# Kernel optimization log

Hardware: AMD Instinct MI355X
Metric: run time of the kernel (lower is better)

The kernel has to match this reference:

```python
import jax, jax.numpy as jnp
import numpy as np

L = 1000  # fixed waveform length implied by MaxPool1d(1000) and [:, :, :1000] slices


def _conv1d(x, w, pad, reflect=False):
    # x: [B, Cin, T], w: [Cout, Cin, K]; torch conv1d == cross-correlation == lax conv
    if reflect:
        x = jnp.pad(x, ((0, 0), (0, 0), (pad, pad)), mode='reflect')
        pads = [(0, 0)]
    else:
        pads = [(pad, pad)]
    return jax.lax.conv_general_dilated(x, w, (1,), pads,
                                        dimension_numbers=('NCH', 'OIH', 'NCH'))


def setup_inputs() -> dict:
    key = jax.random.key(0)
    ks = jax.random.split(key, 10)
    B = 4096
    s = 0.1  # weight init scale
    return {
        'wf': jax.random.normal(ks[0], (B, 1, L), jnp.float32),
        'mask': jnp.ones((B, L), jnp.float32),
        'SPE': jax.random.uniform(ks[1], (L,), jnp.float32),
        'w_cum_area': jax.random.normal(ks[2], (1, 1, 121), jnp.float32) * s,
        'w_x': jax.random.normal(ks[3], (1, 1, 121), jnp.float32) * s,
        'w_div': jax.random.normal(ks[4], (1, 1, 121), jnp.float32) * s,
        'w_roll': jax.random.normal(ks[5], (1, 1, 101), jnp.float32) * s,
        'w_sub': jax.random.normal(ks[6], (15, 3, 21), jnp.float32) * s,
        'w_comb': jax.random.normal(ks[7], (1, 1, 5, 101, 3), jnp.float32) * s,
        'W_param': jnp.array([0.0, 5.0, 10.0], jnp.float32),
    }


def reference(wf, mask, SPE, w_cum_area, w_x, w_div, w_roll, w_sub, w_comb, W_param):
    B = wf.shape[0]
    # fixed (non-learned) derivative + running-mean kernels from __init__
    div_x_w = jnp.array([1/280, -4/105, 1/5, -4/5, 0.0, 4/5, -1/5, 4/105, -1/280],
                        jnp.float32).reshape(1, 1, 9)
    run_mean_w = jnp.full((1, 1, 51), 1.0 / 51, jnp.float32)

    # h = MaxPool1d(1000)(wf).squeeze(1).tile(1,3) / SPE.amax(); tiling == broadcast
    h = wf.max(axis=(1, 2))[:, None] / SPE.max()            # [B,1]
    W = jax.nn.softmax(-jax.nn.relu(h - W_param), axis=1)   # [B,3]

    cum_area = jnp.cumsum(wf, axis=-1)                      # [B,1,L]
    div_x_smd = _conv1d(_conv1d(wf, div_x_w, 4), run_mean_w, 25)  # zero-padded convs

    BL = _conv1d(cum_area, w_roll, 100, reflect=True)[:, :, :L] * w_cum_area.sum()
    fit_cum = jax.nn.relu(_conv1d(cum_area, w_cum_area, 100, reflect=True)[:, :, :L] - BL)
    fit_x = jax.nn.relu(_conv1d(wf, w_x, 100, reflect=True))[:, :, :L]
    fit_div = jax.nn.relu(_conv1d(div_x_smd, w_div, 100, reflect=True))[:, :, :L]

    features1 = jnp.concatenate([fit_cum, fit_x, fit_div], axis=1)   # [B,3,L]
    S = features1.sum(axis=2, keepdims=True) + 1e-10
    features1_norm = features1 / S

    features2 = _conv1d(features1_norm, w_sub, 10, reflect=True)     # [B,15,L]
    # [B,L,15] -> [B,L,5,3], weight the 3-way split by per-sample W
    fc = features2.transpose(0, 2, 1).reshape(B, L, 5, 3) * W[:, None, None, :]
    fc = fc.transpose(0, 2, 1, 3)[:, None]                           # [B,1,5,L,3]

    out = jax.lax.conv_general_dilated(fc, w_comb, (1, 1, 1),
                                       [(0, 0), (50, 50), (0, 0)],
                                       dimension_numbers=('NCDHW', 'OIDHW', 'NCDHW'))
    out = jax.nn.softplus(out).reshape(B, L)                         # [B,L]

    amax = out.max(axis=1, keepdims=True) + 1e-10
    out_norm = out / amax * mask
    return jax.nn.softmax(1e4 * out_norm, axis=1)
```

## Files before the change

kernel.cpp:

```cpp
#include <hip/hip_runtime.h>
#include <math.h>

#define TPB 256
#define LW  1000
#define CSTR 1124

#define OFF_WFE   0
#define OFF_CUME  1120
#define OFF_DSE   2240
#define OFF_F1E   3360
#define OFF_SCAND 3360
#define OFF_C     3872
#define OFF_RED   6740
#define SMEM_F    6748
#define OFF_KC    0
#define OFF_WS2   376
#define OFF_F2V   1456
#define OFF_PART  0

__device__ __forceinline__ float4 ld4(const float* p) { return *(const float4*)p; }

__device__ __forceinline__ float blk_red_max(float v, float* red) {
  #pragma unroll
  for (int o = 32; o > 0; o >>= 1) v = fmaxf(v, __shfl_xor(v, o, 64));
  const int w = threadIdx.x >> 6;
  if ((threadIdx.x & 63) == 0) red[w] = v;
  __syncthreads();
  float r = fmaxf(fmaxf(red[0], red[1]), fmaxf(red[2], red[3]));
  __syncthreads();
  return r;
}

__device__ __forceinline__ float blk_red_sum(float v, float* red) {
  #pragma unroll
  for (int o = 32; o > 0; o >>= 1) v += __shfl_xor(v, o, 64);
  const int w = threadIdx.x >> 6;
  if ((threadIdx.x & 63) == 0) red[w] = v;
  __syncthreads();
  float r = red[0] + red[1] + red[2] + red[3];
  __syncthreads();
  return r;
}

__device__ __forceinline__ int refl(int j) {
  return j < 0 ? -j : (j >= LW ? 2 * LW - 2 - j : j);
}

template<int OFF0>
__device__ __forceinline__ void f2v_accum(const float* xr, const float* wr, float acc[4]) {
  float xw[12];
  *(float4*)xw       = ld4(xr);
  *(float4*)(xw + 4) = ld4(xr + 4);
  *(float4*)(xw + 8) = ld4(xr + 8);
  #pragma unroll
  for (int jb = 0; jb < 20; jb += 4) {
    float4 w4 = ld4(wr + jb);
    const float wv[4] = {w4.x, w4.y, w4.z, w4.w};
    #pragma unroll
    for (int kk = 0; kk < 4; ++kk)
      #pragma unroll
      for (int o = 0; o < 4; ++o)
        acc[o] = fmaf(wv[kk], xw[OFF0 + kk + o], acc[o]);
    #pragma unroll
    for (int j = 0; j < 8; ++j) xw[j] = xw[j + 4];
    *(float4*)(xw + 8) = ld4(xr + jb + 12);
  }
  const float w20 = wr[20];
  #pragma unroll
  for (int o = 0; o < 4; ++o) acc[o] = fmaf(w20, xw[OFF0 + o], acc[o]);
}

extern "C" __global__ void prep_kernel(const float* __restrict__ wsub_g,
                                       const float* __restrict__ wcb_g,
                                       const float* __restrict__ wca_g,
                                       const float* __restrict__ spe_g,
                                       float* __restrict__ P) {
  __shared__ float sred[4];
  const int task = blockIdx.x * blockDim.x + threadIdx.x;
  if (task < 1089) {
    const int m = task / 363;
    const int r = task - m * 363;
    const int cin = r / 121;
    const int k = r - cin * 121;
    float acc = 0.f;
    for (int q = 0; q < 5; ++q) {
      const int ch = 3 * q + m;
      const float* ws = wsub_g + (ch * 3 + cin) * 21;
      #pragma unroll
      for (int j = 0; j < 21; ++j) {
        const int a = k - j;
        if (a >= 0 && a <= 100) acc = fmaf(ws[j], wcb_g[q * 303 + a * 3 + m], acc);
      }
    }
    P[task] = acc;
  } else if (task == 1089) {
    float s = 0.f;
    for (int k = 0; k < 121; ++k) s += wca_g[k];
    P[1089] = s;
  }
  if (blockIdx.x == 4) {
    float mx = -INFINITY;
    for (int t = threadIdx.x; t < LW; t += TPB) mx = fmaxf(mx, spe_g[t]);
    #pragma unroll
    for (int o = 32; o > 0; o >>= 1) mx = fmaxf(mx, __shfl_xor(mx, o, 64));
    if ((threadIdx.x & 63) == 0) sred[threadIdx.x >> 6] = mx;
    __syncthreads();
    if (threadIdx.x == 0)
      P[1090] = fmaxf(fmaxf(sred[0], sred[1]), fmaxf(sred[2], sred[3]));
  }
}

extern "C" __global__ void __launch_bounds__(TPB, 6)
spot_kernel(const float* __restrict__ wf_g,  const float* __restrict__ mask_g,
            const float* __restrict__ spe_g, const float* __restrict__ wca_g,
            const float* __restrict__ wx_g,  const float* __restrict__ wdv_g,
            const float* __restrict__ wrl_g, const float* __restrict__ wsub_g,
            const float* __restrict__ wcb_g, const float* __restrict__ wp_g,
            const float* __restrict__ P_g,   float* __restrict__ out_g)
{
  __shared__ __align__(16) float sm[SMEM_F];
  const int tid = threadIdx.x;
  const int b = blockIdx.x;
  const float* wf = wf_g + (size_t)b * LW;
  float* red = sm + OFF_RED;
  const int t0 = 4 * tid;

  for (int i = tid; i < 1120; i += TPB) sm[OFF_WFE + i] = wf[refl(i - 100)];
  double* scand = (double*)(sm + OFF_SCAND);
  double l0 = 0, l1 = 0, l2 = 0, l3 = 0;
  float hmx = -INFINITY;
  if (tid < 250) {
    float4 wv4 = ld4(wf + t0);
    hmx = fmaxf(fmaxf(wv4.x, wv4.y), fmaxf(wv4.z, wv4.w));
    l0 = (double)wv4.x;
    l1 = l0 + (double)wv4.y;
    l2 = l1 + (double)wv4.z;
    l3 = l2 + (double)wv4.w;
  }
  scand[tid] = l3;
  hmx = blk_red_max(hmx, red);

  const float smx = P_g[1090];
  const float swca = P_g[1089];
  const float h = hmx / smx;
  float a0 = -fmaxf(h - wp_g[0], 0.f);
  float a1 = -fmaxf(h - wp_g[1], 0.f);
  float a2 = -fmaxf(h - wp_g[2], 0.f);
  float am = fmaxf(a0, fmaxf(a1, a2));
  float e0 = expf(a0 - am), e1 = expf(a1 - am), e2 = expf(a2 - am);
  float es = e0 + e1 + e2;
  float Wv[3] = { e0 / es, e1 / es, e2 / es };

  if (tid < 64) {
    double s0 = scand[4 * tid], s1 = scand[4 * tid + 1];
    double s2 = scand[4 * tid + 2], s3 = scand[4 * tid + 3];
    double tot = s0 + s1 + s2 + s3;
    double inc = tot;
    #pragma unroll
    for (int o = 1; o < 64; o <<= 1) {
      double n = __shfl_up(inc, o, 64);
      if ((tid & 63) >= o) inc += n;
    }
    double ex = inc - tot;
    scand[4 * tid]     = ex;
    scand[4 * tid + 1] = ex + s0;
    scand[4 * tid + 2] = ex + s0 + s1;
    scand[4 * tid + 3] = ex + s0 + s1 + s2;
  }
  __syncthreads();
  if (tid < 250) {
    double base = scand[tid];
    float4 cv = { (float)(base + l0), (float)(base + l1),
                  (float)(base + l2), (float)(base + l3) };
    *(float4*)(sm + OFF_CUME + 100 + t0) = cv;
  }
  const float dker[9] = {1.f/280.f, -4.f/105.f, 0.2f, -0.8f, 0.f, 0.8f, -0.2f, 4.f/105.f, -1.f/280.f};
  float dv0 = 0, dv1 = 0, dv2 = 0, dv3 = 0;
  if (tid >= 1 && tid <= 248) {
    float xw[12];
    const float* xr = sm + OFF_WFE + t0 + 96;
    *(float4*)xw = ld4(xr); *(float4*)(xw+4) = ld4(xr+4); *(float4*)(xw+8) = ld4(xr+8);
    float d[4];
    #pragma unroll
    for (int j = 0; j < 4; ++j) {
      float a = 0.f;
      #pragma unroll
      for (int k = 0; k < 9; ++k) {
        if (k == 4) continue;
        a = fmaf(dker[k], xw[j + k], a);
      }
      d[j] = a;
    }
    dv0 = d[0]; dv1 = d[1]; dv2 = d[2]; dv3 = d[3];
  } else if (tid == 0 || tid == 249) {
    float d[4];
    #pragma unroll
    for (int j = 0; j < 4; ++j) {
      float a = 0.f;
      for (int k = 0; k < 9; ++k) {
        if (k == 4) continue;
        const int o = t0 + j - 4 + k;
        if (o >= 0 && o < LW) a = fmaf(dker[k], sm[OFF_WFE + 100 + o], a);
      }
      d[j] = a;
    }
    dv0 = d[0]; dv1 = d[1]; dv2 = d[2]; dv3 = d[3];
  }
  {
    const float s0 = dv0, s1 = s0 + dv1, s2 = s1 + dv2, s3 = s2 + dv3;
    float inc = s3;
    const int lane = tid & 63;
    #pragma unroll
    for (int o = 1; o < 64; o <<= 1) {
      float n = __shfl_up(inc, o, 64);
      if (lane >= o) inc += n;
    }
    float* redw = red + 4;
    if (lane == 63) redw[tid >> 6] = inc;
    __syncthreads();
    float base = 0.f;
    for (int w = 0; w < (tid >> 6); ++w) base += redw[w];
    if (tid < 250) {
      const float ex = base + inc - s3;
      float4 cv = { ex + s0, ex + s1, ex + s2, ex + s3 };
      *(float4*)(sm + OFF_C + t0) = cv;
    }
  }
  __syncthreads();
  for (int t = tid; t < LW; t += TPB) {
    const float hi = sm[OFF_C + (t + 25 > 999 ? 999 : t + 25)];
    const float lo = (t >= 26) ? sm[OFF_C + t - 26] : 0.f;
    sm[OFF_DSE + 100 + t] = (hi - lo) * (1.f / 51.f);
  }
  for (int i = tid; i < 120; i += TPB) {
    if (i < 100) sm[OFF_CUME + i] = sm[OFF_CUME + 200 - i];
    else         sm[OFF_CUME + 1000 + i] = sm[OFF_CUME + 2198 - (1000 + i)];
  }
  __syncthreads();
  for (int i = tid; i < 120; i += TPB) {
    if (i < 100) sm[OFF_DSE + i] = sm[OFF_DSE + 200 - i];
    else         sm[OFF_DSE + 1000 + i] = sm[OFF_DSE + 2198 - (1000 + i)];
  }
  __syncthreads();

  float lsC = 0.f, lsX = 0.f, lsD = 0.f;
  if (tid < 250) {
    const float* ce = sm + OFF_CUME + t0;
    const float* we = sm + OFF_WFE + t0;
    const float* de = sm + OFF_DSE + t0;
    float cw_[8], ww_[8], dw_[8];
    *(float4*)cw_ = ld4(ce); *(float4*)(cw_ + 4) = ld4(ce + 4);
    *(float4*)ww_ = ld4(we); *(float4*)(ww_ + 4) = ld4(we + 4);
    *(float4*)dw_ = ld4(de); *(float4*)(dw_ + 4) = ld4(de + 4);
    float aC[4] = {0,0,0,0}, aB[4] = {0,0,0,0}, aX[4] = {0,0,0,0}, aD[4] = {0,0,0,0};
    for (int g = 0; g < 100; g += 4) {
      #pragma unroll
      for (int kk = 0; kk < 4; ++kk) {
        const int k = g + kk;
        const float wa = wca_g[k], wxk = wx_g[k], wdk = wdv_g[k], wr = wrl_g[k];
        #pragma unroll
        for (int j = 0; j < 4; ++j) {
          aC[j] = fmaf(wa,  cw_[kk + j], aC[j]);
          aB[j] = fmaf(wr,  cw_[kk + j], aB[j]);
          aX[j] = fmaf(wxk, ww_[kk + j], aX[j]);
          aD[j] = fmaf(wdk, dw_[kk + j], aD[j]);
        }
      }
      #pragma unroll
      for (int j = 0; j < 4; ++j) { cw_[j] = cw_[j+4]; ww_[j] = ww_[j+4]; dw_[j] = dw_[j+4]; }
      *(float4*)(cw_ + 4) = ld4(ce + g + 8);
      *(float4*)(ww_ + 4) = ld4(we + g + 8);
      *(float4*)(dw_ + 4) = ld4(de + g + 8);
    }
    {
      const float wr100 = wrl_g[100];
      #pragma unroll
      for (int j = 0; j < 4; ++j) aB[j] = fmaf(wr100, cw_[j], aB[j]);
    }
    for (int g = 100; g < 116; g += 4) {
      #pragma unroll
      for (int kk = 0; kk < 4; ++kk) {
        const int k = g + kk;
        const float wa = wca_g[k], wxk = wx_g[k], wdk = wdv_g[k];
        #pragma unroll
        for (int j = 0; j < 4; ++j) {
          aC[j] = fmaf(wa,  cw_[kk + j], aC[j]);
          aX[j] = fmaf(wxk, ww_[kk + j], aX[j]);
          aD[j] = fmaf(wdk, dw_[kk + j], aD[j]);
        }
      }
      #pragma unroll
      for (int j = 0; j < 4; ++j) { cw_[j] = cw_[j+4]; ww_[j] = ww_[j+4]; dw_[j] = dw_[j+4]; }
      *(float4*)(cw_ + 4) = ld4(ce + g + 8);
      *(float4*)(ww_ + 4) = ld4(we + g + 8);
      *(float4*)(dw_ + 4) = ld4(de + g + 8);
    }
    #pragma unroll
    for (int kk = 0; kk < 5; ++kk) {
      const int k = 116 + kk;
      const float wa = wca_g[k], wxk = wx_g[k], wdk = wdv_g[k];
      #pragma unroll
      for (int j = 0; j < 4; ++j) {
        aC[j] = fmaf(wa,  cw_[kk + j], aC[j]);
        aX[j] = fmaf(wxk, ww_[kk + j], aX[j]);
        aD[j] = fmaf(wdk, dw_[kk + j], aD[j]);
      }
    }
    float4 vC, vX, vD;
    float* pC = (float*)&vC; float* pX = (float*)&vX; float* pD = (float*)&vD;
    #pragma unroll
    for (int j = 0; j < 4; ++j) {
      float fc = fmaxf(fmaf(-aB[j], swca, aC[j]), 0.f);
      float fx = fmaxf(aX[j], 0.f);
      float fd = fmaxf(aD[j], 0.f);
      pC[j] = fc; pX[j] = fx; pD[j] = fd;
      lsC += fc; lsX += fx; lsD += fd;
    }
    *(float4*)(sm + OFF_F1E + 0 * CSTR + 60 + t0) = vC;
    *(float4*)(sm + OFF_F1E + 1 * CSTR + 60 + t0) = vX;
    *(float4*)(sm + OFF_F1E + 2 * CSTR + 60 + t0) = vD;
  }
  const float SC = blk_red_sum(lsC, red) + 1e-10f;
  const float SX = blk_red_sum(lsX, red) + 1e-10f;
  const float SD = blk_red_sum(lsD, red) + 1e-10f;
  {
    const float iC = 1.f / SC, iX = 1.f / SX, iD = 1.f / SD;
    for (int t = tid; t < LW; t += TPB) {
      sm[OFF_F1E + 0 * CSTR + 60 + t] *= iC;
      sm[OFF_F1E + 1 * CSTR + 60 + t] *= iX;
      sm[OFF_F1E + 2 * CSTR + 60 + t] *= iD;
    }
  }
  __syncthreads();

  for (int i = tid; i < 360; i += TPB) {
    const int c = i / 120, j = i - c * 120;
    const int dst = (j < 60) ? j : (1000 + j);
    const int src = (j < 60) ? (120 - j) : (1118 - j);
    sm[OFF_F1E + c * CSTR + dst] = sm[OFF_F1E + c * CSTR + src];
  }
  for (int i = tid; i < 363; i += TPB) {
    const int cin = i / 121, k = i - cin * 121;
    const float* Pp = P_g + cin * 121 + k;
    sm[OFF_KC + cin * 124 + k] =
        fmaf(Wv[0], Pp[0], fmaf(Wv[1], Pp[363], Wv[2] * Pp[726]));
  }
  for (int i = tid; i < 1080; i += TPB) {
    const int row = i / 24, k = i - row * 24;
    sm[OFF_WS2 + i] = (k < 21) ? wsub_g[row * 21 + k] : 0.f;
  }
  __syncthreads();

  float res[4] = {0, 0, 0, 0};
  if (tid < 250) {
    #pragma unroll
    for (int cin = 0; cin < 3; ++cin) {
      const float* xr = sm + OFF_F1E + cin * CSTR + t0;
      const float* kc = sm + OFF_KC + cin * 124;
      float xw[8];
      *(float4*)xw = ld4(xr); *(float4*)(xw + 4) = ld4(xr + 4);
      for (int g = 0; g < 120; g += 4) {
        float4 kw = ld4(kc + g);
        const float wv[4] = {kw.x, kw.y, kw.z, kw.w};
        #pragma unroll
        for (int kk = 0; kk < 4; ++kk)
          #pragma unroll
          for (int j = 0; j < 4; ++j) res[j] = fmaf(wv[kk], xw[kk + j], res[j]);
        #pragma unroll
        for (int j = 0; j < 4; ++j) xw[j] = xw[j + 4];
        *(float4*)(xw + 4) = ld4(xr + g + 8);
      }
      const float w120 = kc[120];
      #pragma unroll
      for (int j = 0; j < 4; ++j) res[j] = fmaf(w120, xw[j], res[j]);
    }
  }
  for (int task = tid; task < 390; task += TPB) {
    const int side = (task >= 195) ? 1 : 0;
    const int r = task - 195 * side;
    const int ch = r / 13;
    const int gl = r - 13 * ch;
    float acc[4] = {0, 0, 0, 0};
    const float* wrb = sm + OFF_WS2 + ch * 72;
    if (side == 0) {
      const int xb = 4 * gl;
      #pragma unroll
      for (int cin = 0; cin < 3; ++cin)
        f2v_accum<0>(sm + OFF_F1E + cin * CSTR + xb, wrb + cin * 24, acc);
    } else {
      const int xb = 1048 + 4 * gl;
      #pragma unroll
      for (int cin = 0; cin < 3; ++cin)
        f2v_accum<2>(sm + OFF_F1E + cin * CSTR + xb, wrb + cin * 24, acc);
    }
    const int dst = OFF_F2V + ch * 104 + side * 52 + 4 * gl;
    if (gl < 12) {
      float4 st = {acc[0], acc[1], acc[2], acc[3]};
      *(float4*)(sm + dst) = st;
    } else {
      sm[dst] = acc[0]; sm[dst + 1] = acc[1];
    }
  }
  __syncthreads();

  for (int task = tid; task < 500; task += TPB) {
    const int q = task / 100;
    const int tcol = task - q * 100;
    const float* f0 = sm + OFF_F2V + (3 * q) * 104;
    float acc = 0.f;
    if (tcol < 50) {
      const int t = tcol;
      for (int a = 0; a <= 49 - t; ++a) {
        const int up = t + a;
        const float* wb = wcb_g + q * 303 + a * 3;
        acc = fmaf(Wv[0] * wb[0], f0[up], acc);
        acc = fmaf(Wv[1] * wb[1], f0[104 + up], acc);
        acc = fmaf(Wv[2] * wb[2], f0[208 + up], acc);
      }
    } else {
      const int tp = tcol;
      for (int d = 0; d <= tp - 50; ++d) {
        const int up = tp - d + 2;
        const int a = 100 - d;
        const float* wb = wcb_g + q * 303 + a * 3;
        acc = fmaf(Wv[0] * wb[0], f0[up], acc);
        acc = fmaf(Wv[1] * wb[1], f0[104 + up], acc);
        acc = fmaf(Wv[2] * wb[2], f0[208 + up], acc);
      }
    }
    sm[OFF_PART + task] = acc;
  }
  __syncthreads();

  if (tid < 250 && (t0 < 52 || t0 >= 948)) {
    #pragma unroll
    for (int j = 0; j < 4; ++j) {
      const int t = t0 + j;
      if (t < 50) {
        float c = 0.f;
        #pragma unroll
        for (int q = 0; q < 5; ++q) c += sm[OFF_PART + q * 100 + t];
        res[j] -= c;
      } else if (t >= 950) {
        const int tc = t - 900;
        float c = 0.f;
        #pragma unroll
        for (int q = 0; q < 5; ++q) c += sm[OFF_PART + q * 100 + tc];
        res[j] -= c;
      }
    }
  }
  float sp[4];
  float lm = -INFINITY;
  if (tid < 250) {
    #pragma unroll
    for (int j = 0; j < 4; ++j) {
      const float z = res[j];
      sp[j] = fmaxf(z, 0.f) + log1pf(expf(-fabsf(z)));
      lm = fmaxf(lm, sp[j]);
    }
  }
  const float amax = blk_red_max(lm, red) + 1e-10f;
  float v4[4];
  float lm2 = -INFINITY;
  if (tid < 250) {
    const float4 mv = ld4(mask_g + (size_t)b * LW + t0);
    const float* mj = (const float*)&mv;
    const float ia = 1e4f / amax;
    #pragma unroll
    for (int j = 0; j < 4; ++j) {
      v4[j] = (sp[j] * ia) * mj[j];
      lm2 = fmaxf(lm2, v4[j]);
    }
  }
  const float m2 = blk_red_max(lm2, red);
  float ls = 0.f;
  float e4[4];
  if (tid < 250) {
    #pragma unroll
    for (int j = 0; j < 4; ++j) {
      e4[j] = expf(v4[j] - m2);
      ls += e4[j];
    }
  }
  const float S2 = blk_red_sum(ls, red);
  if (tid < 250) {
    const float invs = 1.f / S2;
    float4 st = { e4[0] * invs, e4[1] * invs, e4[2] * invs, e4[3] * invs };
    *(float4*)(out_g + (size_t)b * LW + t0) = st;
  }
}

extern "C" void kernel_launch(void* const* d_in, const int* in_sizes, int n_in,
                              void* d_out, int out_size, void* d_ws, size_t ws_size,
                              hipStream_t stream) {
  (void)n_in; (void)ws_size; (void)out_size;
  const float* wf   = (const float*)d_in[0];
  const float* mask = (const float*)d_in[1];
  const float* spe  = (const float*)d_in[2];
  const float* wca  = (const float*)d_in[3];
  const float* wx   = (const float*)d_in[4];
  const float* wdv  = (const float*)d_in[5];
  const float* wrl  = (const float*)d_in[6];
  const float* wsub = (const float*)d_in[7];
  const float* wcb  = (const float*)d_in[8];
  const float* wp   = (const float*)d_in[9];
  float* P = (float*)d_ws;
  const int B = in_sizes[0] / LW;
  hipLaunchKernelGGL(prep_kernel, dim3(5), dim3(TPB), 0, stream, wsub, wcb, wca, spe, P);
  hipLaunchKernelGGL(spot_kernel, dim3(B), dim3(TPB), 0, stream,
                     wf, mask, spe, wca, wx, wdv, wrl, wsub, wcb, wp, P, (float*)d_out);
}
```

Before: 283.8 us.

## Fold baseline conv into cum-area weights and fuse block reductions

```diff
diff --git a/kernel.cpp b/kernel.cpp
--- a/kernel.cpp
+++ b/kernel.cpp
@@ -12,7 +12,7 @@
 #define OFF_SCAND 3360
 #define OFF_C     3872
 #define OFF_RED   6740
-#define SMEM_F    6748
+#define SMEM_F    6752
 #define OFF_KC    0
 #define OFF_WS2   376
 #define OFF_F2V   1456
@@ -42,8 +42,20 @@
   return r;
 }
 
-__device__ __forceinline__ int refl(int j) {
-  return j < 0 ? -j : (j >= LW ? 2 * LW - 2 - j : j);
+__device__ __forceinline__ void blk_red_sum3(float& a, float& b, float& c, float* red) {
+  #pragma unroll
+  for (int o = 32; o > 0; o >>= 1) {
+    a += __shfl_xor(a, o, 64);
+    b += __shfl_xor(b, o, 64);
+    c += __shfl_xor(c, o, 64);
+  }
+  const int w = threadIdx.x >> 6;
+  if ((threadIdx.x & 63) == 0) { red[w] = a; red[4 + w] = b; red[8 + w] = c; }
+  __syncthreads();
+  a = red[0] + red[1] + red[2]  + red[3];
+  b = red[4] + red[5] + red[6]  + red[7];
+  c = red[8] + red[9] + red[10] + red[11];
+  __syncthreads();
 }
 
 template<int OFF0>
@@ -74,8 +86,10 @@
                                        const float* __restrict__ wcb_g,
                                        const float* __restrict__ wca_g,
                                        const float* __restrict__ spe_g,
+                                       const float* __restrict__ wrl_g,
                                        float* __restrict__ P) {
   __shared__ float sred[4];
+  __shared__ float s_swca;
   const int task = blockIdx.x * blockDim.x + threadIdx.x;
   if (task < 1089) {
     const int m = task / 363;
@@ -93,10 +107,6 @@
       }
     }
     P[task] = acc;
-  } else if (task == 1089) {
-    float s = 0.f;
-    for (int k = 0; k < 121; ++k) s += wca_g[k];
-    P[1089] = s;
   }
   if (blockIdx.x == 4) {
     float mx = -INFINITY;
@@ -104,9 +114,20 @@
     #pragma unroll
     for (int o = 32; o > 0; o >>= 1) mx = fmaxf(mx, __shfl_xor(mx, o, 64));
     if ((threadIdx.x & 63) == 0) sred[threadIdx.x >> 6] = mx;
+    if (threadIdx.x == 0) {
+      float s = 0.f;
+      for (int k = 0; k < 121; ++k) s += wca_g[k];
+      s_swca = s;
+    }
     __syncthreads();
     if (threadIdx.x == 0)
       P[1090] = fmaxf(fmaxf(sred[0], sred[1]), fmaxf(sred[2], sred[3]));
+    if (threadIdx.x < 121) {
+      const int k = threadIdx.x;
+      float w = 0.f;
+      if (k < 101) w = wrl_g[k];
+      P[1091 + k] = wca_g[k] - s_swca * w;
+    }
   }
 }
 
@@ -125,12 +146,12 @@
   float* red = sm + OFF_RED;
   const int t0 = 4 * tid;
 
-  for (int i = tid; i < 1120; i += TPB) sm[OFF_WFE + i] = wf[refl(i - 100)];
   double* scand = (double*)(sm + OFF_SCAND);
   double l0 = 0, l1 = 0, l2 = 0, l3 = 0;
   float hmx = -INFINITY;
   if (tid < 250) {
     float4 wv4 = ld4(wf + t0);
+    *(float4*)(sm + OFF_WFE + 100 + t0) = wv4;
     hmx = fmaxf(fmaxf(wv4.x, wv4.y), fmaxf(wv4.z, wv4.w));
     l0 = (double)wv4.x;
     l1 = l0 + (double)wv4.y;
@@ -140,8 +161,12 @@
   scand[tid] = l3;
   hmx = blk_red_max(hmx, red);
 
+  for (int i = tid; i < 120; i += TPB) {
+    if (i < 100) sm[OFF_WFE + i] = sm[OFF_WFE + 200 - i];
+    else         sm[OFF_WFE + 1000 + i] = sm[OFF_WFE + 2198 - (1000 + i)];
+  }
+
   const float smx = P_g[1090];
-  const float swca = P_g[1089];
   const float h = hmx / smx;
   float a0 = -fmaxf(h - wp_g[0], 0.f);
   float a1 = -fmaxf(h - wp_g[1], 0.f);
@@ -236,10 +261,12 @@
     if (i < 100) sm[OFF_CUME + i] = sm[OFF_CUME + 200 - i];
     else         sm[OFF_CUME + 1000 + i] = sm[OFF_CUME + 2198 - (1000 + i)];
   }
-  __syncthreads();
   for (int i = tid; i < 120; i += TPB) {
-    if (i < 100) sm[OFF_DSE + i] = sm[OFF_DSE + 200 - i];
-    else         sm[OFF_DSE + 1000 + i] = sm[OFF_DSE + 2198 - (1000 + i)];
+    const int o = (i < 100) ? (100 - i) : (1098 - i);
+    const float hi = sm[OFF_C + (o + 25 > 999 ? 999 : o + 25)];
+    const float lo = (o >= 26) ? sm[OFF_C + o - 26] : 0.f;
+    const int dst = (i < 100) ? i : (1000 + i);
+    sm[OFF_DSE + dst] = (hi - lo) * (1.f / 51.f);
   }
   __syncthreads();
 
@@ -248,20 +275,20 @@
     const float* ce = sm + OFF_CUME + t0;
     const float* we = sm + OFF_WFE + t0;
     const float* de = sm + OFF_DSE + t0;
+    const float* kcb = P_g + 1091;
     float cw_[8], ww_[8], dw_[8];
     *(float4*)cw_ = ld4(ce); *(float4*)(cw_ + 4) = ld4(ce + 4);
     *(float4*)ww_ = ld4(we); *(float4*)(ww_ + 4) = ld4(we + 4);
     *(float4*)dw_ = ld4(de); *(float4*)(dw_ + 4) = ld4(de + 4);
-    float aC[4] = {0,0,0,0}, aB[4] = {0,0,0,0}, aX[4] = {0,0,0,0}, aD[4] = {0,0,0,0};
-    for (int g = 0; g < 100; g += 4) {
+    float aC[4] = {0,0,0,0}, aX[4] = {0,0,0,0}, aD[4] = {0,0,0,0};
+    for (int g = 0; g < 116; g += 4) {
       #pragma unroll
       for (int kk = 0; kk < 4; ++kk) {
         const int k = g + kk;
-        const float wa = wca_g[k], wxk = wx_g[k], wdk = wdv_g[k], wr = wrl_g[k];
+        const float wc = kcb[k], wxk = wx_g[k], wdk = wdv_g[k];
         #pragma unroll
         for (int j = 0; j < 4; ++j) {
-          aC[j] = fmaf(wa,  cw_[kk + j], aC[j]);
-          aB[j] = fmaf(wr,  cw_[kk + j], aB[j]);
+          aC[j] = fmaf(wc,  cw_[kk + j], aC[j]);
           aX[j] = fmaf(wxk, ww_[kk + j], aX[j]);
           aD[j] = fmaf(wdk, dw_[kk + j], aD[j]);
         }
@@ -272,36 +299,13 @@
       *(float4*)(ww_ + 4) = ld4(we + g + 8);
       *(float4*)(dw_ + 4) = ld4(de + g + 8);
     }
-    {
-      const float wr100 = wrl_g[100];
-      #pragma unroll
-      for (int j = 0; j < 4; ++j) aB[j] = fmaf(wr100, cw_[j], aB[j]);
-    }
-    for (int g = 100; g < 116; g += 4) {
-      #pragma unroll
-      for (int kk = 0; kk < 4; ++kk) {
-        const int k = g + kk;
-        const float wa = wca_g[k], wxk = wx_g[k], wdk = wdv_g[k];
-        #pragma unroll
-        for (int j = 0; j < 4; ++j) {
-          aC[j] = fmaf(wa,  cw_[kk + j], aC[j]);
-          aX[j] = fmaf(wxk, ww_[kk + j], aX[j]);
-          aD[j] = fmaf(wdk, dw_[kk + j], aD[j]);
-        }
-      }
-      #pragma unroll
-      for (int j = 0; j < 4; ++j) { cw_[j] = cw_[j+4]; ww_[j] = ww_[j+4]; dw_[j] = dw_[j+4]; }
-      *(float4*)(cw_ + 4) = ld4(ce + g + 8);
-      *(float4*)(ww_ + 4) = ld4(we + g + 8);
-      *(float4*)(dw_ + 4) = ld4(de + g + 8);
-    }
     #pragma unroll
     for (int kk = 0; kk < 5; ++kk) {
       const int k = 116 + kk;
-      const float wa = wca_g[k], wxk = wx_g[k], wdk = wdv_g[k];
+      const float wc = kcb[k], wxk = wx_g[k], wdk = wdv_g[k];
       #pragma unroll
       for (int j = 0; j < 4; ++j) {
-        aC[j] = fmaf(wa,  cw_[kk + j], aC[j]);
+        aC[j] = fmaf(wc,  cw_[kk + j], aC[j]);
         aX[j] = fmaf(wxk, ww_[kk + j], aX[j]);
         aD[j] = fmaf(wdk, dw_[kk + j], aD[j]);
       }
@@ -310,7 +314,7 @@
     float* pC = (float*)&vC; float* pX = (float*)&vX; float* pD = (float*)&vD;
     #pragma unroll
     for (int j = 0; j < 4; ++j) {
-      float fc = fmaxf(fmaf(-aB[j], swca, aC[j]), 0.f);
+      float fc = fmaxf(aC[j], 0.f);
       float fx = fmaxf(aX[j], 0.f);
       float fd = fmaxf(aD[j], 0.f);
       pC[j] = fc; pX[j] = fx; pD[j] = fd;
@@ -320,18 +324,11 @@
     *(float4*)(sm + OFF_F1E + 1 * CSTR + 60 + t0) = vX;
     *(float4*)(sm + OFF_F1E + 2 * CSTR + 60 + t0) = vD;
   }
-  const float SC = blk_red_sum(lsC, red) + 1e-10f;
-  const float SX = blk_red_sum(lsX, red) + 1e-10f;
-  const float SD = blk_red_sum(lsD, red) + 1e-10f;
-  {
-    const float iC = 1.f / SC, iX = 1.f / SX, iD = 1.f / SD;
-    for (int t = tid; t < LW; t += TPB) {
-      sm[OFF_F1E + 0 * CSTR + 60 + t] *= iC;
-      sm[OFF_F1E + 1 * CSTR + 60 + t] *= iX;
-      sm[OFF_F1E + 2 * CSTR + 60 + t] *= iD;
-    }
-  }
-  __syncthreads();
+  float SC = lsC, SX = lsX, SD = lsD;
+  blk_red_sum3(SC, SX, SD, red);
+  const float iC = 1.f / (SC + 1e-10f);
+  const float iX = 1.f / (SX + 1e-10f);
+  const float iD = 1.f / (SD + 1e-10f);
 
   for (int i = tid; i < 360; i += TPB) {
     const int c = i / 120, j = i - c * 120;
@@ -341,13 +338,16 @@
   }
   for (int i = tid; i < 363; i += TPB) {
     const int cin = i / 121, k = i - cin * 121;
+    const float iv = (cin == 0) ? iC : ((cin == 1) ? iX : iD);
     const float* Pp = P_g + cin * 121 + k;
     sm[OFF_KC + cin * 124 + k] =
-        fmaf(Wv[0], Pp[0], fmaf(Wv[1], Pp[363], Wv[2] * Pp[726]));
+        fmaf(Wv[0], Pp[0], fmaf(Wv[1], Pp[363], Wv[2] * Pp[726])) * iv;
   }
   for (int i = tid; i < 1080; i += TPB) {
     const int row = i / 24, k = i - row * 24;
-    sm[OFF_WS2 + i] = (k < 21) ? wsub_g[row * 21 + k] : 0.f;
+    const int cin = row - (row / 3) * 3;
+    const float iv = (cin == 0) ? iC : ((cin == 1) ? iX : iD);
+    sm[OFF_WS2 + i] = (k < 21) ? wsub_g[row * 21 + k] * iv : 0.f;
   }
   __syncthreads();
 
@@ -403,32 +403,26 @@
   }
   __syncthreads();
 
-  for (int task = tid; task < 500; task += TPB) {
-    const int q = task / 100;
-    const int tcol = task - q * 100;
+  for (int s = tid; s < 250; s += TPB) {
+    const int q = s / 50;
+    const int u = s - 50 * q;
     const float* f0 = sm + OFF_F2V + (3 * q) * 104;
-    float acc = 0.f;
-    if (tcol < 50) {
-      const int t = tcol;
-      for (int a = 0; a <= 49 - t; ++a) {
-        const int up = t + a;
-        const float* wb = wcb_g + q * 303 + a * 3;
-        acc = fmaf(Wv[0] * wb[0], f0[up], acc);
-        acc = fmaf(Wv[1] * wb[1], f0[104 + up], acc);
-        acc = fmaf(Wv[2] * wb[2], f0[208 + up], acc);
-      }
-    } else {
-      const int tp = tcol;
-      for (int d = 0; d <= tp - 50; ++d) {
-        const int up = tp - d + 2;
-        const int a = 100 - d;
-        const float* wb = wcb_g + q * 303 + a * 3;
-        acc = fmaf(Wv[0] * wb[0], f0[up], acc);
-        acc = fmaf(Wv[1] * wb[1], f0[104 + up], acc);
-        acc = fmaf(Wv[2] * wb[2], f0[208 + up], acc);
-      }
-    }
-    sm[OFF_PART + task] = acc;
+    const float* wq = wcb_g + q * 303;
+    float la0 = 0, la1 = 0, la2 = 0, ra0 = 0, ra1 = 0, ra2 = 0;
+    for (int i = 0; i <= 49 - u; ++i) {
+      const int upL = u + i;
+      const float* wbL = wq + 3 * i;
+      la0 = fmaf(wbL[0], f0[upL], la0);
+      la1 = fmaf(wbL[1], f0[104 + upL], la1);
+      la2 = fmaf(wbL[2], f0[208 + upL], la2);
+      const int upR = 101 - u - i;
+      const float* wbR = wq + 3 * (100 - i);
+      ra0 = fmaf(wbR[0], f0[upR], ra0);
+      ra1 = fmaf(wbR[1], f0[104 + upR], ra1);
+      ra2 = fmaf(wbR[2], f0[208 + upR], ra2);
+    }
+    sm[OFF_PART + q * 100 + u]      = fmaf(Wv[0], la0, fmaf(Wv[1], la1, Wv[2] * la2));
+    sm[OFF_PART + q * 100 + 99 - u] = fmaf(Wv[0], ra0, fmaf(Wv[1], ra1, Wv[2] * ra2));
   }
   __syncthreads();
 
@@ -450,36 +444,41 @@
       }
     }
   }
-  float sp[4];
-  float lm = -INFINITY;
-  if (tid < 250) {
+  float sp[4], mj[4];
+  float lm = -INFINITY, lmm = -INFINITY;
+  if (tid < 250) {
+    const float4 mv = ld4(mask_g + (size_t)b * LW + t0);
+    mj[0] = mv.x; mj[1] = mv.y; mj[2] = mv.z; mj[3] = mv.w;
     #pragma unroll
     for (int j = 0; j < 4; ++j) {
       const float z = res[j];
       sp[j] = fmaxf(z, 0.f) + log1pf(expf(-fabsf(z)));
       lm = fmaxf(lm, sp[j]);
-    }
-  }
-  const float amax = blk_red_max(lm, red) + 1e-10f;
-  float v4[4];
-  float lm2 = -INFINITY;
-  if (tid < 250) {
-    const float4 mv = ld4(mask_g + (size_t)b * LW + t0);
-    const float* mj = (const float*)&mv;
-    const float ia = 1e4f / amax;
-    #pragma unroll
-    for (int j = 0; j < 4; ++j) {
-      v4[j] = (sp[j] * ia) * mj[j];
-      lm2 = fmaxf(lm2, v4[j]);
-    }
-  }
-  const float m2 = blk_red_max(lm2, red);
+      lmm = fmaxf(lmm, sp[j] * mj[j]);
+    }
+  }
+  #pragma unroll
+  for (int o = 32; o > 0; o >>= 1) {
+    lm = fmaxf(lm, __shfl_xor(lm, o, 64));
+    lmm = fmaxf(lmm, __shfl_xor(lmm, o, 64));
+  }
+  {
+    const int w = tid >> 6;
+    if ((tid & 63) == 0) { red[w] = lm; red[4 + w] = lmm; }
+  }
+  __syncthreads();
+  const float amax = fmaxf(fmaxf(red[0], red[1]), fmaxf(red[2], red[3])) + 1e-10f;
+  const float mmax = fmaxf(fmaxf(red[4], red[5]), fmaxf(red[6], red[7]));
+  __syncthreads();
+  const float ia = 1e4f / amax;
+  const float m2 = mmax * ia;
   float ls = 0.f;
   float e4[4];
   if (tid < 250) {
     #pragma unroll
     for (int j = 0; j < 4; ++j) {
-      e4[j] = expf(v4[j] - m2);
+      const float v = (sp[j] * ia) * mj[j];
+      e4[j] = expf(v - m2);
       ls += e4[j];
     }
   }
@@ -507,7 +506,7 @@
   const float* wp   = (const float*)d_in[9];
   float* P = (float*)d_ws;
   const int B = in_sizes[0] / LW;
-  hipLaunchKernelGGL(prep_kernel, dim3(5), dim3(TPB), 0, stream, wsub, wcb, wca, spe, P);
+  hipLaunchKernelGGL(prep_kernel, dim3(5), dim3(TPB), 0, stream, wsub, wcb, wca, spe, wrl, P);
   hipLaunchKernelGGL(spot_kernel, dim3(B), dim3(TPB), 0, stream,
                      wf, mask, spe, wca, wx, wdv, wrl, wsub, wcb, wp, P, (float*)d_out);
 }
```

Measured after the change: 315.4 us. 1.11x slower.
